# Performance work log

Measured on AMD Instinct MI355X. Metric: run time of the kernel, lower is better.

The kernel has to match this reference:

```python
import jax, jax.numpy as jnp
import numpy as np

B, NPB, M, K, F = 4, 8192, 2048, 64, 64   # clouds, points/cloud, fps samples/cloud, max neighbors, feat dim
RADIUS = 0.2
MLP_DIMS = (F + 3, 64, 64, 128)           # local_nn: concat(x_j, pos_j - pos_i) -> 128


def setup_inputs() -> dict:
    key = jax.random.key(0)
    ks = jax.random.split(key, 8)
    N = B * NPB
    x = jax.random.normal(ks[0], (N, F), jnp.float32)
    pos = jax.random.uniform(ks[1], (N, 3), jnp.float32)  # unit cube
    batch = jnp.repeat(jnp.arange(B, dtype=jnp.int32), NPB)
    inp = {"x": x, "pos": pos, "batch": batch}
    for i in range(3):
        din, dout = MLP_DIMS[i], MLP_DIMS[i + 1]
        inp[f"W{i+1}"] = jax.random.normal(ks[2 + i], (din, dout), jnp.float32) / np.sqrt(din)
        inp[f"b{i+1}"] = jnp.zeros((dout,), jnp.float32)
    return inp


def _fps(pos_b):
    """Farthest point sampling on one cloud. pos_b: [n,3] -> [M] indices (start at point 0)."""
    d0 = jnp.sum((pos_b - pos_b[0]) ** 2, axis=-1)  # [n]
    def body(min_d, _):
        idx = jnp.argmax(min_d)
        d = jnp.sum((pos_b - pos_b[idx]) ** 2, axis=-1)
        return jnp.minimum(min_d, d), idx
    _, idxs = jax.lax.scan(body, d0, None, length=M - 1)
    return jnp.concatenate([jnp.zeros((1,), idxs.dtype), idxs])


def _sa_one_cloud(x_b, pos_b, W1, b1, W2, b2, W3, b3):
    samp = _fps(pos_b)                 # [M]
    pos_s = pos_b[samp]                # [M,3]
    # radius-ball query, capped at K nearest inside the ball (centers are in pos so self is always hit)
    d2 = jnp.sum((pos_s[:, None, :] - pos_b[None, :, :]) ** 2, axis=-1)  # [M,n]
    score = jnp.where(d2 <= RADIUS * RADIUS, -d2, -jnp.inf)
    vals, nbr = jax.lax.top_k(score, K)            # [M,K]
    valid = jnp.isfinite(vals)                     # [M,K]
    # PointConv message: MLP(concat(x_j, pos_j - pos_i)), then max-pool over neighbors
    feat = jnp.concatenate([x_b[nbr], pos_b[nbr] - pos_s[:, None, :]], axis=-1)  # [M,K,F+3]
    h = jax.nn.relu(feat @ W1 + b1)
    h = jax.nn.relu(h @ W2 + b2)
    h = jax.nn.relu(h @ W3 + b3)                   # [M,K,128]
    h = jnp.where(valid[:, :, None], h, -jnp.inf)
    return jnp.max(h, axis=1), samp                # [M,128], [M]


def reference(x, pos, batch, W1, b1, W2, b2, W3, b3):
    xb = x.reshape(B, NPB, F)
    pb = pos.reshape(B, NPB, 3)
    out, samp = jax.vmap(lambda xx, pp: _sa_one_cloud(xx, pp, W1, b1, W2, b2, W3, b3))(xb, pb)
    pos_out = jnp.take_along_axis(pb, samp[:, :, None], axis=1)       # [B,M,3]
    batch_out = jnp.repeat(jnp.arange(B, dtype=batch.dtype), M)       # [B*M]
    return out.reshape(B * M, -1), pos_out.reshape(B * M, 3), batch_out
```

## Files before the change

### kernel.cpp

```cpp
#include <hip/hip_runtime.h>

typedef unsigned int u32;
typedef unsigned long long u64;
typedef float f32x2 __attribute__((ext_vector_type(2)));

#define NPB 8192
#define BCL 4
#define MS 2048
#define KN 64
#define OFF_POS   (BCL * MS * 128)
#define OFF_BATCH (OFF_POS + BCL * MS * 3)
#define SMEM_BYTES (NPB * 16 + 32 + MS * 4)

__device__ inline u64 umax64(u64 a, u64 b) { return a < b ? b : a; }
__device__ inline u32 umax32(u32 a, u32 b) { return a < b ? b : a; }

__device__ inline f32x2 pk_add(f32x2 a, f32x2 b) {
  f32x2 d;
  asm("v_pk_add_f32 %0, %1, %2" : "=v"(d) : "v"(a), "v"(b));
  return d;
}
__device__ inline f32x2 pk_mul(f32x2 a, f32x2 b) {
  f32x2 d;
  asm("v_pk_mul_f32 %0, %1, %2" : "=v"(d) : "v"(a), "v"(b));
  return d;
}

__device__ inline u32 wave_max_u32(u32 v) {
  v = umax32(v, (u32)__builtin_amdgcn_update_dpp(0, (int)v, 0x111, 0xf, 0xf, false));
  v = umax32(v, (u32)__builtin_amdgcn_update_dpp(0, (int)v, 0x112, 0xf, 0xf, false));
  v = umax32(v, (u32)__builtin_amdgcn_update_dpp(0, (int)v, 0x114, 0xf, 0xf, false));
  v = umax32(v, (u32)__builtin_amdgcn_update_dpp(0, (int)v, 0x118, 0xf, 0xf, false));
  v = umax32(v, (u32)__builtin_amdgcn_update_dpp(0, (int)v, 0x142, 0xa, 0xf, false));
  v = umax32(v, (u32)__builtin_amdgcn_update_dpp(0, (int)v, 0x143, 0xc, 0xf, false));
  return (u32)__builtin_amdgcn_readlane((int)v, 63);
}
__device__ inline u64 wave_max_key(u64 lkey) {
  u32 hi = (u32)(lkey >> 32), lo32v = (u32)lkey;
  u32 m = wave_max_u32(hi);
  u32 c = wave_max_u32(hi == m ? lo32v : 0u);
  return ((u64)m << 32) | c;
}

__device__ inline u32 part1by2(u32 x) {
  x &= 0x3ffu;
  x = (x | (x << 16)) & 0x030000FFu;
  x = (x | (x << 8))  & 0x0300F00Fu;
  x = (x | (x << 4))  & 0x030C30C3u;
  x = (x | (x << 2))  & 0x09249249u;
  return x;
}

__global__ __launch_bounds__(1024) void init_ready(u32* __restrict__ ready) {
  int i = blockIdx.x * 1024 + threadIdx.x;
  if (i < BCL * MS) ready[i] = 0u;
}

__global__ __launch_bounds__(1024) void pipeline_kernel(
    const float* __restrict__ x, const float* __restrict__ pos,
    u32* __restrict__ ready,
    const float* __restrict__ W1, const float* __restrict__ b1,
    const float* __restrict__ W2, const float* __restrict__ b2,
    const float* __restrict__ W3, const float* __restrict__ b3,
    float* __restrict__ out) {
  __shared__ __align__(16) unsigned char smem_raw[SMEM_BYTES];
  int t = threadIdx.x;

  if (blockIdx.x < BCL) {
    u64* sortb = (u64*)smem_raw;
    float4* tab = (float4*)smem_raw;
    u64* slot = (u64*)(smem_raw + NPB * 16);
    int* s_samp = (int*)(smem_raw + NPB * 16 + 32);

    int b = blockIdx.x, lane = t & 63;
    const float* pb = pos + (size_t)b * NPB * 3;

    if (t == 1) atomicExch(&ready[(size_t)b * MS], 1u);

    for (int i = t; i < NPB; i += 1024) {
      float xx = pb[i * 3], yy = pb[i * 3 + 1], zz = pb[i * 3 + 2];
      u32 xi = (u32)fminf(fmaxf(xx * 1024.0f, 0.0f), 1023.0f);
      u32 yi = (u32)fminf(fmaxf(yy * 1024.0f, 0.0f), 1023.0f);
      u32 zi = (u32)fminf(fmaxf(zz * 1024.0f, 0.0f), 1023.0f);
      u32 m = (part1by2(zi) << 2) | (part1by2(yi) << 1) | part1by2(xi);
      sortb[i] = ((u64)m << 13) | (u32)i;
    }
    for (int k = 2; k <= NPB; k <<= 1) {
      for (int j = k >> 1; j > 0; j >>= 1) {
        __syncthreads();
        for (int i = t; i < NPB; i += 1024) {
          int ix = i ^ j;
          if (ix > i) {
            u64 a = sortb[i], c = sortb[ix];
            bool up = ((i & k) == 0);
            if ((a > c) == up) { sortb[i] = c; sortb[ix] = a; }
          }
        }
      }
    }
    __syncthreads();
    int oi[8];
    #pragma unroll
    for (int i = 0; i < 8; ++i) oi[i] = (int)(sortb[8 * t + i] & 0x1FFFu);
    __syncthreads();

    for (int i = t; i < NPB; i += 1024) {
      float xx = pb[i * 3], yy = pb[i * 3 + 1], zz = pb[i * 3 + 2];
      tab[i] = float4{xx, yy, zz, 0.0f};
    }
    if (t < 3) slot[t] = 0;
    if (t == 0) s_samp[0] = 0;
    __syncthreads();

    f32x2 px[4], py[4], pz[4], mind[4];
    u32 lo[8];
    float bxl = 1e30f, bxh = -1e30f, byl = 1e30f, byh = -1e30f, bzl = 1e30f, bzh = -1e30f;
    #pragma unroll
    for (int j = 0; j < 4; ++j) {
      int iA = oi[2 * j], iB = oi[2 * j + 1];
      float4 A = tab[iA], B = tab[iB];
      px[j] = f32x2{A.x, B.x}; py[j] = f32x2{A.y, B.y}; pz[j] = f32x2{A.z, B.z};
      lo[2 * j] = ~(u32)iA; lo[2 * j + 1] = ~(u32)iB;
      bxl = fminf(bxl, fminf(A.x, B.x)); bxh = fmaxf(bxh, fmaxf(A.x, B.x));
      byl = fminf(byl, fminf(A.y, B.y)); byh = fmaxf(byh, fmaxf(A.y, B.y));
      bzl = fminf(bzl, fminf(A.z, B.z)); bzh = fmaxf(bzh, fmaxf(A.z, B.z));
    }
    u64 lkey = 0, wkey;
    {
      float4 c0 = tab[0];
      f32x2 mcx = f32x2{-c0.x, -c0.x}, mcy = f32x2{-c0.y, -c0.y}, mcz = f32x2{-c0.z, -c0.z};
      #pragma unroll
      for (int j = 0; j < 4; ++j) {
        f32x2 dx = pk_add(px[j], mcx), dy = pk_add(py[j], mcy), dz = pk_add(pz[j], mcz);
        mind[j] = pk_add(pk_add(pk_mul(dx, dx), pk_mul(dy, dy)), pk_mul(dz, dz));
        u64 kA = ((u64)__float_as_uint(mind[j].x) << 32) | lo[2 * j];
        u64 kB = ((u64)__float_as_uint(mind[j].y) << 32) | lo[2 * j + 1];
        lkey = umax64(lkey, umax64(kA, kB));
      }
      wkey = wave_max_key(lkey);
    }

    int cur = 0, nxt = 1;
    for (int it = 1; it < MS; ++it) {
      if (lane == 0) atomicMax((u64*)&slot[cur], wkey);
      if (t == 64) slot[nxt] = 0;
      __syncthreads();
      u64 g = slot[cur];
      int win = (int)(~(u32)g) & (NPB - 1);
      if (t == 0) s_samp[it] = win;
      if (t == 65) atomicExch(&ready[(size_t)b * MS + it], (u32)(win + 1));
      float4 wc = tab[win];
      float ncx = wc.x, ncy = wc.y, ncz = wc.z;
      float lmax = __uint_as_float((u32)(lkey >> 32));
      float ax = fmaxf(fmaxf(__fsub_rn(bxl, ncx), __fsub_rn(ncx, bxh)), 0.0f);
      float ay = fmaxf(fmaxf(__fsub_rn(byl, ncy), __fsub_rn(ncy, byh)), 0.0f);
      float az = fmaxf(fmaxf(__fsub_rn(bzl, ncz), __fsub_rn(ncz, bzh)), 0.0f);
      float lb2 = (ax * ax + ay * ay + az * az) * 0.9999961853f;
      bool upd = (lb2 <= lmax);
      if (__ballot(upd)) {
        if (upd) {
          f32x2 mcx = f32x2{-ncx, -ncx}, mcy = f32x2{-ncy, -ncy}, mcz = f32x2{-ncz, -ncz};
          u64 acc = 0;
          #pragma unroll
          for (int j = 0; j < 4; ++j) {
            f32x2 dx = pk_add(px[j], mcx), dy = pk_add(py[j], mcy), dz = pk_add(pz[j], mcz);
            f32x2 d2 = pk_add(pk_add(pk_mul(dx, dx), pk_mul(dy, dy)), pk_mul(dz, dz));
            mind[j].x = fminf(mind[j].x, d2.x);
            mind[j].y = fminf(mind[j].y, d2.y);
            u64 kA = ((u64)__float_as_uint(mind[j].x) << 32) | lo[2 * j];
            u64 kB = ((u64)__float_as_uint(mind[j].y) << 32) | lo[2 * j + 1];
            acc = umax64(acc, umax64(kA, kB));
          }
          lkey = acc;
        }
        wkey = wave_max_key(lkey);
      }
      cur = nxt;
      nxt = nxt + 1 == 3 ? 0 : nxt + 1;
    }
    __syncthreads();
    float* pos_out = out + OFF_POS + (size_t)b * MS * 3;
    float* batch_out = out + OFF_BATCH + (size_t)b * MS;
    for (int m = t; m < MS; m += 1024) {
      int s = s_samp[m];
      float4 c = tab[s];
      pos_out[m * 3] = c.x;
      pos_out[m * 3 + 1] = c.y;
      pos_out[m * 3 + 2] = c.z;
      batch_out[m] = (float)b;
    }
    return;
  }

  {
    int cblk = blockIdx.x - BCL;
    int b = cblk & (BCL - 1), m = cblk >> 2;
    int c = b * MS + m;
    const float R2CUT = (float)(0.2 * 0.2);

    u64* cand = (u64*)smem_raw;
    int* s_cnt = (int*)(smem_raw + 4096);
    int* s_win = (int*)(smem_raw + 4100);
    float (*s_feat)[68] = (float(*)[68])(smem_raw + 4112);
    float (*s_h)[68]    = (float(*)[68])(smem_raw + 4112 + 17408);
    float (*s_w)[64]    = (float(*)[64])(smem_raw + 4112 + 34816);
    float* s_mask       = (float*)(smem_raw + 4112 + 52224);
    float (*s_red)[64]  = (float(*)[64])(smem_raw + 4112 + 52480);

    const float* pb = pos + (size_t)b * NPB * 3;

    if (t == 0) {
      u32 v;
      while ((v = atomicAdd(&ready[c], 0u)) == 0u) __builtin_amdgcn_s_sleep(8);
      *s_win = (int)(v - 1u);
      *s_cnt = 0;
    }
    __syncthreads();
    int s = *s_win;
    float cx = pb[s * 3], cy = pb[s * 3 + 1], cz = pb[s * 3 + 2];

    if (t < 256) {
      for (int j = t; j < NPB; j += 256) {
        float dx = __fsub_rn(pb[j * 3], cx);
        float dy = __fsub_rn(pb[j * 3 + 1], cy);
        float dz = __fsub_rn(pb[j * 3 + 2], cz);
        float d2 = __fadd_rn(__fadd_rn(__fmul_rn(dx, dx), __fmul_rn(dy, dy)), __fmul_rn(dz, dz));
        if (d2 <= R2CUT) {
          int sl = atomicAdd(s_cnt, 1);
          if (sl < 512) cand[sl] = ((u64)__float_as_uint(d2) << 32) | (u32)j;
        }
      }
    }
    __syncthreads();
    int n = *s_cnt; if (n > 512) n = 512;
    if (t < 256) {
      for (int i = t; i < 512; i += 256) if (i >= n) cand[i] = ~0ull;
    }
    __syncthreads();
    for (int k = 2; k <= 512; k <<= 1) {
      for (int j = k >> 1; j > 0; j >>= 1) {
        if (t < 256) {
          for (int i = t; i < 512; i += 256) {
            int ix = i ^ j;
            if (ix > i) {
              u64 a = cand[i], bb = cand[ix];
              bool up = ((i & k) == 0);
              if ((a > bb) == up) { cand[i] = bb; cand[ix] = a; }
            }
          }
        }
        __syncthreads();
      }
    }

    if (t < 256) {
      int r = t >> 2, q = t & 3;
      int j = (r < n) ? (int)(cand[r] & 0xffffffffu) : -1;
      bool valid = (j >= 0 && j < NPB);
      size_t jj = valid ? (size_t)j : 0;
      const float4* xp = (const float4*)(x + ((size_t)b * NPB + jj) * 64 + q * 16);
      float4 v[4];
      for (int i = 0; i < 4; ++i) v[i] = xp[i];
      for (int i = 0; i < 4; ++i) {
        s_feat[r][q * 16 + i * 4 + 0] = valid ? v[i].x : 0.0f;
        s_feat[r][q * 16 + i * 4 + 1] = valid ? v[i].y : 0.0f;
        s_feat[r][q * 16 + i * 4 + 2] = valid ? v[i].z : 0.0f;
        s_feat[r][q * 16 + i * 4 + 3] = valid ? v[i].w : 0.0f;
      }
    }
    if (t < 64) {
      int r = t;
      int j = (r < n) ? (int)(cand[r] & 0xffffffffu) : -1;
      bool valid = (j >= 0 && j < NPB);
      s_mask[r] = valid ? 0.0f : -__builtin_inff();
      size_t jj = valid ? (size_t)j : (size_t)s;
      for (int d = 0; d < 3; ++d) {
        float pj = pos[((size_t)b * NPB + jj) * 3 + d];
        float pc = pos[((size_t)b * NPB + s) * 3 + d];
        s_feat[r][64 + d] = __fsub_rn(pj, pc);
      }
    }
    if (t < 256) {
      for (int idx = t; idx < 67 * 64; idx += 256)
        s_w[idx >> 6][idx & 63] = W1[idx];
    }
    __syncthreads();

    {
      int r = t >> 2, n0 = (t & 3) * 16;
      float acc[16];
      if (t < 256) {
        for (int j = 0; j < 16; ++j) acc[j] = b1[n0 + j];
        for (int k = 0; k < 67; ++k) {
          float f = s_feat[r][k];
          for (int j = 0; j < 16; ++j) acc[j] += f * s_w[k][n0 + j];
        }
      }
      __syncthreads();
      if (t < 256) {
        for (int j = 0; j < 16; ++j) s_h[r][n0 + j] = fmaxf(acc[j], 0.0f);
        for (int idx = t; idx < 64 * 64; idx += 256)
          s_w[idx >> 6][idx & 63] = W2[idx];
      }
    }
    __syncthreads();

    {
      int r = t >> 2, n0 = (t & 3) * 16;
      float acc[16];
      if (t < 256) {
        for (int j = 0; j < 16; ++j) acc[j] = b2[n0 + j];
        for (int k = 0; k < 64; ++k) {
          float f = s_h[r][k];
          for (int j = 0; j < 16; ++j) acc[j] += f * s_w[k][n0 + j];
        }
      }
      __syncthreads();
      if (t < 256) {
        for (int j = 0; j < 16; ++j) s_feat[r][n0 + j] = fmaxf(acc[j], 0.0f);
      }
    }
    __syncthreads();

    for (int h = 0; h < 2; ++h) {
      if (t < 256) {
        for (int idx = t; idx < 64 * 64; idx += 256)
          s_w[idx >> 6][idx & 63] = W3[(size_t)(idx >> 6) * 128 + h * 64 + (idx & 63)];
      }
      __syncthreads();
      if (t < 256) {
        int n2 = t & 63, rg = t >> 6;
        float acc[16];
        float bias = b3[h * 64 + n2];
        for (int rr = 0; rr < 16; ++rr) acc[rr] = bias;
        for (int k = 0; k < 64; ++k) {
          float w = s_w[k][n2];
          for (int rr = 0; rr < 16; ++rr) acc[rr] += s_feat[rg * 16 + rr][k] * w;
        }
        float mm = -__builtin_inff();
        for (int rr = 0; rr < 16; ++rr)
          mm = fmaxf(mm, fmaxf(acc[rr], 0.0f) + s_mask[rg * 16 + rr]);
        s_red[rg][n2] = mm;
      }
      __syncthreads();
      if (t < 64) {
        float mm = fmaxf(fmaxf(s_red[0][t], s_red[1][t]), fmaxf(s_red[2][t], s_red[3][t]));
        out[(size_t)c * 128 + h * 64 + t] = mm;
      }
      __syncthreads();
    }
  }
}

extern "C" void kernel_launch(void* const* d_in, const int* in_sizes, int n_in,
                              void* d_out, int out_size, void* d_ws, size_t ws_size,
                              hipStream_t stream) {
  const float* x   = (const float*)d_in[0];
  const float* pos = (const float*)d_in[1];
  const float* W1 = (const float*)d_in[3];
  const float* b1 = (const float*)d_in[4];
  const float* W2 = (const float*)d_in[5];
  const float* b2 = (const float*)d_in[6];
  const float* W3 = (const float*)d_in[7];
  const float* b3 = (const float*)d_in[8];

  float* out = (float*)d_out;
  u32* ready = (u32*)d_ws;

  init_ready<<<(BCL * MS + 1023) / 1024, 1024, 0, stream>>>(ready);
  pipeline_kernel<<<BCL + BCL * MS, 1024, 0, stream>>>(
      x, pos, ready, W1, b1, W2, b2, W3, b3, out);
}
```

Baseline: 1.652 ms.

## Pack three consumer centers per block using idle thread groups

Consumer blocks previously used only 256 of their 1024 threads for one sample center. Each block now handles three centers, one per 256-thread group, with private shared-memory regions and a single weight buffer shared by all groups. Weight loads now use the whole block. This cuts the consumer block count by about a factor of three and puts the idle threads to work, but the three groups are tied together by barriers. A group whose center becomes ready late will stall the other two, and total shared memory per block grows.

```diff
diff --git a/kernel.cpp b/kernel.cpp
--- a/kernel.cpp
+++ b/kernel.cpp
@@ -8,9 +8,12 @@
 #define BCL 4
 #define MS 2048
 #define KN 64
+#define TOTC (BCL * MS)
 #define OFF_POS   (BCL * MS * 128)
 #define OFF_BATCH (OFF_POS + BCL * MS * 3)
 #define SMEM_BYTES (NPB * 16 + 32 + MS * 4)
+#define GRP_PRIV 40208
+#define CONS_BLKS ((TOTC + 2) / 3)
 
 __device__ inline u64 umax64(u64 a, u64 b) { return a < b ? b : a; }
 __device__ inline u32 umax32(u32 a, u32 b) { return a < b ? b : a; }
@@ -53,7 +56,7 @@
 
 __global__ __launch_bounds__(1024) void init_ready(u32* __restrict__ ready) {
   int i = blockIdx.x * 1024 + threadIdx.x;
-  if (i < BCL * MS) ready[i] = 0u;
+  if (i < TOTC) ready[i] = 0u;
 }
 
 __global__ __launch_bounds__(1024) void pipeline_kernel(
@@ -194,33 +197,43 @@
 
   {
     int cblk = blockIdx.x - BCL;
-    int b = cblk & (BCL - 1), m = cblk >> 2;
+    int g = t >> 8;
+    int tl = t & 255;
+    bool work = (g < 3);
+    int p = 3 * cblk + (work ? g : 0);
+    if (p >= TOTC) p = TOTC - 1;
+    int b = p & (BCL - 1), m = p >> 2;
     int c = b * MS + m;
     const float R2CUT = (float)(0.2 * 0.2);
 
-    u64* cand = (u64*)smem_raw;
-    int* s_cnt = (int*)(smem_raw + 4096);
-    int* s_win = (int*)(smem_raw + 4100);
-    float (*s_feat)[68] = (float(*)[68])(smem_raw + 4112);
-    float (*s_h)[68]    = (float(*)[68])(smem_raw + 4112 + 17408);
-    float (*s_w)[64]    = (float(*)[64])(smem_raw + 4112 + 34816);
-    float* s_mask       = (float*)(smem_raw + 4112 + 52224);
-    float (*s_red)[64]  = (float(*)[64])(smem_raw + 4112 + 52480);
+    float (*s_w)[64] = (float(*)[64])(smem_raw);
+    unsigned char* gb = smem_raw + 17408 + (work ? g : 0) * GRP_PRIV;
+    u64* cand = (u64*)gb;
+    int* s_cnt = (int*)(gb + 4096);
+    int* s_win = (int*)(gb + 4100);
+    float (*s_feat)[68] = (float(*)[68])(gb + 4112);
+    float (*s_h)[68]    = (float(*)[68])(gb + 21520);
+    float* s_mask       = (float*)(gb + 38928);
+    float (*s_red)[64]  = (float(*)[64])(gb + 39184);
 
     const float* pb = pos + (size_t)b * NPB * 3;
 
-    if (t == 0) {
+    if (work && tl == 0) {
       u32 v;
       while ((v = atomicAdd(&ready[c], 0u)) == 0u) __builtin_amdgcn_s_sleep(8);
       *s_win = (int)(v - 1u);
       *s_cnt = 0;
     }
     __syncthreads();
-    int s = *s_win;
-    float cx = pb[s * 3], cy = pb[s * 3 + 1], cz = pb[s * 3 + 2];
-
-    if (t < 256) {
-      for (int j = t; j < NPB; j += 256) {
+    int s = 0;
+    float cx = 0.0f, cy = 0.0f, cz = 0.0f;
+    if (work) {
+      s = *s_win;
+      cx = pb[s * 3]; cy = pb[s * 3 + 1]; cz = pb[s * 3 + 2];
+    }
+
+    if (work) {
+      for (int j = tl; j < NPB; j += 256) {
         float dx = __fsub_rn(pb[j * 3], cx);
         float dy = __fsub_rn(pb[j * 3 + 1], cy);
         float dz = __fsub_rn(pb[j * 3 + 2], cz);
@@ -232,15 +245,16 @@
       }
     }
     __syncthreads();
-    int n = *s_cnt; if (n > 512) n = 512;
-    if (t < 256) {
-      for (int i = t; i < 512; i += 256) if (i >= n) cand[i] = ~0ull;
+    int n = 0;
+    if (work) {
+      n = *s_cnt; if (n > 512) n = 512;
+      for (int i = tl; i < 512; i += 256) if (i >= n) cand[i] = ~0ull;
     }
     __syncthreads();
     for (int k = 2; k <= 512; k <<= 1) {
       for (int j = k >> 1; j > 0; j >>= 1) {
-        if (t < 256) {
-          for (int i = t; i < 512; i += 256) {
+        if (work) {
+          for (int i = tl; i < 512; i += 256) {
             int ix = i ^ j;
             if (ix > i) {
               u64 a = cand[i], bb = cand[ix];
@@ -253,8 +267,8 @@
       }
     }
 
-    if (t < 256) {
-      int r = t >> 2, q = t & 3;
+    if (work) {
+      int r = tl >> 2, q = tl & 3;
       int j = (r < n) ? (int)(cand[r] & 0xffffffffu) : -1;
       bool valid = (j >= 0 && j < NPB);
       size_t jj = valid ? (size_t)j : 0;
@@ -268,8 +282,8 @@
         s_feat[r][q * 16 + i * 4 + 3] = valid ? v[i].w : 0.0f;
       }
     }
-    if (t < 64) {
-      int r = t;
+    if (work && tl < 64) {
+      int r = tl;
       int j = (r < n) ? (int)(cand[r] & 0xffffffffu) : -1;
       bool valid = (j >= 0 && j < NPB);
       s_mask[r] = valid ? 0.0f : -__builtin_inff();
@@ -280,16 +294,14 @@
         s_feat[r][64 + d] = __fsub_rn(pj, pc);
       }
     }
-    if (t < 256) {
-      for (int idx = t; idx < 67 * 64; idx += 256)
-        s_w[idx >> 6][idx & 63] = W1[idx];
-    }
+    for (int idx = t; idx < 67 * 64; idx += 1024)
+      s_w[idx >> 6][idx & 63] = W1[idx];
     __syncthreads();
 
     {
-      int r = t >> 2, n0 = (t & 3) * 16;
+      int r = tl >> 2, n0 = (tl & 3) * 16;
       float acc[16];
-      if (t < 256) {
+      if (work) {
         for (int j = 0; j < 16; ++j) acc[j] = b1[n0 + j];
         for (int k = 0; k < 67; ++k) {
           float f = s_feat[r][k];
@@ -297,18 +309,18 @@
         }
       }
       __syncthreads();
-      if (t < 256) {
+      if (work) {
         for (int j = 0; j < 16; ++j) s_h[r][n0 + j] = fmaxf(acc[j], 0.0f);
-        for (int idx = t; idx < 64 * 64; idx += 256)
-          s_w[idx >> 6][idx & 63] = W2[idx];
-      }
+      }
+      for (int idx = t; idx < 64 * 64; idx += 1024)
+        s_w[idx >> 6][idx & 63] = W2[idx];
     }
     __syncthreads();
 
     {
-      int r = t >> 2, n0 = (t & 3) * 16;
+      int r = tl >> 2, n0 = (tl & 3) * 16;
       float acc[16];
-      if (t < 256) {
+      if (work) {
         for (int j = 0; j < 16; ++j) acc[j] = b2[n0 + j];
         for (int k = 0; k < 64; ++k) {
           float f = s_h[r][k];
@@ -316,20 +328,18 @@
         }
       }
       __syncthreads();
-      if (t < 256) {
+      if (work) {
         for (int j = 0; j < 16; ++j) s_feat[r][n0 + j] = fmaxf(acc[j], 0.0f);
       }
     }
     __syncthreads();
 
     for (int h = 0; h < 2; ++h) {
-      if (t < 256) {
-        for (int idx = t; idx < 64 * 64; idx += 256)
-          s_w[idx >> 6][idx & 63] = W3[(size_t)(idx >> 6) * 128 + h * 64 + (idx & 63)];
-      }
-      __syncthreads();
-      if (t < 256) {
-        int n2 = t & 63, rg = t >> 6;
+      for (int idx = t; idx < 64 * 64; idx += 1024)
+        s_w[idx >> 6][idx & 63] = W3[(size_t)(idx >> 6) * 128 + h * 64 + (idx & 63)];
+      __syncthreads();
+      if (work) {
+        int n2 = tl & 63, rg = tl >> 6;
         float acc[16];
         float bias = b3[h * 64 + n2];
         for (int rr = 0; rr < 16; ++rr) acc[rr] = bias;
@@ -343,9 +353,9 @@
         s_red[rg][n2] = mm;
       }
       __syncthreads();
-      if (t < 64) {
-        float mm = fmaxf(fmaxf(s_red[0][t], s_red[1][t]), fmaxf(s_red[2][t], s_red[3][t]));
-        out[(size_t)c * 128 + h * 64 + t] = mm;
+      if (work && tl < 64) {
+        float mm = fmaxf(fmaxf(s_red[0][tl], s_red[1][tl]), fmaxf(s_red[2][tl], s_red[3][tl]));
+        out[(size_t)c * 128 + h * 64 + tl] = mm;
       }
       __syncthreads();
     }
@@ -367,7 +377,7 @@
   float* out = (float*)d_out;
   u32* ready = (u32*)d_ws;
 
-  init_ready<<<(BCL * MS + 1023) / 1024, 1024, 0, stream>>>(ready);
-  pipeline_kernel<<<BCL + BCL * MS, 1024, 0, stream>>>(
+  init_ready<<<(TOTC + 1023) / 1024, 1024, 0, stream>>>(ready);
+  pipeline_kernel<<<BCL + CONS_BLKS, 1024, 0, stream>>>(
       x, pos, ready, W1, b1, W2, b2, W3, b3, out);
 }
```

Result: faster. 1.484 ms (median of 2 runs) (-10.2%).
